# Kernel optimization log

Hardware: AMD Instinct MI355X
Metric: run time of the kernel (lower is better)

Reference implementation:

```python
import jax, jax.numpy as jnp
import numpy as np

N_NODES = 1_000_000
N_EDGES = 16_000_000
D = 2          # num_dimensions (hard-coded in source)
H = 64         # hidden_channnels
G = 1024       # number of graphs in the batch


def setup_inputs() -> dict:
    key = jax.random.key(0)
    ks = jax.random.split(key, 10)
    x = jax.random.normal(ks[0], (N_NODES, D), dtype=jnp.float32)
    edge_index = jax.random.randint(ks[1], (2, N_EDGES), 0, N_NODES, dtype=jnp.int64)
    batch = jnp.sort(jax.random.randint(ks[2], (N_NODES,), 0, G, dtype=jnp.int64))
    s = 0.5
    return {
        "x": x,
        "lin_w": jax.random.normal(ks[3], (D, D), dtype=jnp.float32) * s,
        "lin_b": jnp.zeros((D,), jnp.float32),
        "gn_weight": jnp.ones((D,), jnp.float32),
        "gn_bias": jnp.zeros((D,), jnp.float32),
        "gn_mean_scale": jnp.ones((D,), jnp.float32),
        "gcn_w": jax.random.normal(ks[4], (D, D), dtype=jnp.float32) * s,
        "gcn_b": jnp.zeros((D,), jnp.float32),
        "fc1_w": jax.random.normal(ks[5], (H, D), dtype=jnp.float32) * s,
        "fc1_b": jnp.zeros((H,), jnp.float32),
        "fc2_w": jax.random.normal(ks[6], (D, H), dtype=jnp.float32) * (1.0 / np.sqrt(H)),
        "fc2_b": jnp.zeros((D,), jnp.float32),
        "edge_index": edge_index,
        "batch": batch,
    }


def reference(x, lin_w, lin_b, gn_weight, gn_bias, gn_mean_scale,
              gcn_w, gcn_b, fc1_w, fc1_b, fc2_w, fc2_b, edge_index, batch):
    n = x.shape[0]
    # lin
    h = x @ lin_w.T + lin_b
    # GraphNorm called without batch -> single-graph stats; eps = num_dimensions = 2 (arg-order quirk)
    mean = h.mean(axis=0)
    out = h - mean * gn_mean_scale
    var = (out * out).mean(axis=0)
    h = gn_weight * out * jax.lax.rsqrt(var + jnp.float32(D)) + gn_bias
    h = jax.nn.relu(h)
    # GCNConv (add_self_loops=True, sym norm) + residual
    row, col = edge_index[0], edge_index[1]
    deg = jax.ops.segment_sum(jnp.ones_like(col, dtype=h.dtype), col, num_segments=n) + 1.0
    dis = jax.lax.rsqrt(deg)                       # deg^{-1/2}
    hw = h @ gcn_w.T                               # [N, D]
    msg = (dis[row] * dis[col])[:, None] * hw[row] # [E, D]
    agg = jax.ops.segment_sum(msg, col, num_segments=n)
    conv = agg + hw / deg[:, None] + gcn_b         # self-loop term = dis_i^2 * hw_i
    h = conv + h
    # fc1
    h = h @ fc1_w.T + fc1_b                        # [N, H]
    # InstanceNorm1d on 2D input -> unbatched (C=N, L=H): per-row norm over H; eps = H (arg-order quirk)
    m = h.mean(axis=1, keepdims=True)
    v = ((h - m) ** 2).mean(axis=1, keepdims=True)
    h = (h - m) * jax.lax.rsqrt(v + jnp.float32(H))
    # fc2
    h = h @ fc2_w.T + fc2_b                        # [N, D]
    # scatter_mean over batch
    ssum = jax.ops.segment_sum(h, batch, num_segments=G)
    cnt = jax.ops.segment_sum(jnp.ones((n,), h.dtype), batch, num_segments=G)
    return ssum / jnp.maximum(cnt, 1.0)[:, None]
```

## Files before the change

kernel.cpp:

```cpp
#include <hip/hip_runtime.h>

#define BLK 256
#define CH 8192
#define BSHIFT 12
#define BRANGE 4096
#define BMASK 4095
#define NSB 512


__global__ void k_stats(const float* __restrict__ x, int n, double* __restrict__ partials) {
    float s0 = 0.f, s1 = 0.f, s2 = 0.f, s3 = 0.f, s4 = 0.f;
    int nv = n >> 1;
    int stride = gridDim.x * blockDim.x;
    for (int i = blockIdx.x * blockDim.x + threadIdx.x; i < nv; i += stride) {
        float4 v = reinterpret_cast<const float4*>(x)[i];
        s0 += v.x + v.z; s1 += v.y + v.w;
        s2 += v.x * v.x + v.z * v.z;
        s3 += v.y * v.y + v.w * v.w;
        s4 += v.x * v.y + v.z * v.w;
    }
    if (blockIdx.x == 0 && threadIdx.x == 0 && (n & 1)) {
        float2 v = reinterpret_cast<const float2*>(x)[n - 1];
        s0 += v.x; s1 += v.y; s2 += v.x * v.x; s3 += v.y * v.y; s4 += v.x * v.y;
    }
    for (int off = 32; off; off >>= 1) {
        s0 += __shfl_down(s0, off);
        s1 += __shfl_down(s1, off);
        s2 += __shfl_down(s2, off);
        s3 += __shfl_down(s3, off);
        s4 += __shfl_down(s4, off);
    }
    __shared__ double lds[4][5];
    int wid = threadIdx.x >> 6;
    if ((threadIdx.x & 63) == 0) {
        lds[wid][0] = s0; lds[wid][1] = s1; lds[wid][2] = s2;
        lds[wid][3] = s3; lds[wid][4] = s4;
    }
    __syncthreads();
    if (threadIdx.x == 0) {
        double t0 = 0, t1 = 0, t2 = 0, t3 = 0, t4 = 0;
        for (int w = 0; w < 4; ++w) {
            t0 += lds[w][0]; t1 += lds[w][1]; t2 += lds[w][2];
            t3 += lds[w][3]; t4 += lds[w][4];
        }
        double* o = partials + (size_t)blockIdx.x * 5;
        o[0] = t0; o[1] = t1; o[2] = t2; o[3] = t3; o[4] = t4;
    }
}


__global__ void k_params(const double* __restrict__ partials, int np,
                         const int* __restrict__ bhist, int NB,
                         int* __restrict__ gbase, int* __restrict__ cursor,
                         const float* lin_w, const float* lin_b,
                         const float* gn_w, const float* gn_b, const float* gn_ms,
                         const float* gcn_w, const float* gcn_b,
                         const float* fc1_w, const float* fc1_b,
                         const float* fc2_w, const float* fc2_b,
                         int n, float* __restrict__ P) {
    int tid = threadIdx.x;
    if (bhist) {
        __shared__ int si[256];
        int hv = (tid < NB) ? bhist[tid] : 0;
        si[tid] = hv; __syncthreads();
        for (int off = 1; off < 256; off <<= 1) {
            int t = (tid >= off) ? si[tid - off] : 0;
            __syncthreads();
            si[tid] += t;
            __syncthreads();
        }
        if (tid < NB) { gbase[tid] = si[tid] - hv; cursor[tid] = si[tid] - hv; }
        if (tid == 0) gbase[NB] = si[255];
        __syncthreads();
    }
    double a0 = 0, a1 = 0, a2 = 0, a3 = 0, a4 = 0;
    for (int i = tid; i < np; i += blockDim.x) {
        const double* q = partials + (size_t)i * 5;
        a0 += q[0]; a1 += q[1]; a2 += q[2]; a3 += q[3]; a4 += q[4];
    }
    for (int off = 32; off; off >>= 1) {
        a0 += __shfl_down(a0, off);
        a1 += __shfl_down(a1, off);
        a2 += __shfl_down(a2, off);
        a3 += __shfl_down(a3, off);
        a4 += __shfl_down(a4, off);
    }
    __shared__ double red[4][5];
    int wid = tid >> 6;
    if ((tid & 63) == 0) {
        red[wid][0] = a0; red[wid][1] = a1; red[wid][2] = a2;
        red[wid][3] = a3; red[wid][4] = a4;
    }
    __syncthreads();
    if (tid != 0) return;
    double Sx0 = 0, Sx1 = 0, Sxx = 0, Syy = 0, Sxy = 0;
    for (int w = 0; w < 4; ++w) {
        Sx0 += red[w][0]; Sx1 += red[w][1]; Sxx += red[w][2];
        Syy += red[w][3]; Sxy += red[w][4];
    }
    double N = (double)n;
    for (int c = 0; c < 2; ++c) {
        double L0 = lin_w[c * 2], L1 = lin_w[c * 2 + 1], lb = lin_b[c];
        double m   = (L0 * Sx0 + L1 * Sx1) / N + lb;
        double Eh2 = (L0 * L0 * Sxx + L1 * L1 * Syy + 2.0 * L0 * L1 * Sxy
                      + 2.0 * lb * (L0 * Sx0 + L1 * Sx1)) / N + lb * lb;
        double s   = gn_ms[c];
        double var = Eh2 - 2.0 * s * m * m + s * s * m * m;
        double inv = 1.0 / sqrt(var + 2.0);
        double gam = gn_w[c];
        P[c * 2 + 0] = (float)(gam * inv * L0);
        P[c * 2 + 1] = (float)(gam * inv * L1);
        P[4 + c]     = (float)(gam * inv * (lb - m * s) + gn_b[c]);
    }
    P[6] = gcn_w[0]; P[7] = gcn_w[1]; P[8] = gcn_w[2]; P[9] = gcn_w[3];
    P[10] = gcn_b[0]; P[11] = gcn_b[1];
    double b0 = 0, b1 = 0, bb = 0;
    for (int j = 0; j < 64; ++j) { b0 += fc1_w[2 * j]; b1 += fc1_w[2 * j + 1]; bb += fc1_b[j]; }
    b0 /= 64.0; b1 /= 64.0; bb /= 64.0;
    double S00 = 0, S01 = 0, S11 = 0, Sb0 = 0, Sb1 = 0, Sbb = 0;
    double M00 = 0, M01 = 0, M10 = 0, M11 = 0, t0 = 0, t1 = 0;
    for (int j = 0; j < 64; ++j) {
        double w0 = fc1_w[2 * j] - b0, w1 = fc1_w[2 * j + 1] - b1, b = fc1_b[j] - bb;
        S00 += w0 * w0; S01 += w0 * w1; S11 += w1 * w1;
        Sb0 += w0 * b;  Sb1 += w1 * b;  Sbb += b * b;
        double f0 = fc2_w[j], f1 = fc2_w[64 + j];
        M00 += f0 * w0; M01 += f0 * w1; t0 += f0 * b;
        M10 += f1 * w0; M11 += f1 * w1; t1 += f1 * b;
    }
    P[12] = (float)(S00 / 64.0); P[13] = (float)(S01 / 64.0); P[14] = (float)(S11 / 64.0);
    P[15] = (float)(Sb0 / 64.0); P[16] = (float)(Sb1 / 64.0); P[17] = (float)(Sbb / 64.0);
    P[18] = (float)M00; P[19] = (float)M01; P[20] = (float)M10; P[21] = (float)M11;
    P[22] = (float)t0;  P[23] = (float)t1;
    P[24] = fc2_b[0];   P[25] = fc2_b[1];
}


__global__ void k_hist(const int* __restrict__ col, int E, int NB, int* __restrict__ bhist) {
    __shared__ int h[256];
    for (int j = threadIdx.x; j < 256; j += blockDim.x) h[j] = 0;
    __syncthreads();
    int nq = E >> 2;
    int stride = gridDim.x * blockDim.x;
    for (int q = blockIdx.x * blockDim.x + threadIdx.x; q < nq; q += stride) {
        int4 c = reinterpret_cast<const int4*>(col)[q];
        atomicAdd(&h[c.x >> BSHIFT], 1);
        atomicAdd(&h[c.y >> BSHIFT], 1);
        atomicAdd(&h[c.z >> BSHIFT], 1);
        atomicAdd(&h[c.w >> BSHIFT], 1);
    }
    if (blockIdx.x == 0) {
        for (int e = (nq << 2) + threadIdx.x; e < E; e += blockDim.x)
            atomicAdd(&h[col[e] >> BSHIFT], 1);
    }
    __syncthreads();
    for (int j = threadIdx.x; j < NB; j += blockDim.x)
        if (h[j]) atomicAdd(&bhist[j], h[j]);
}

__global__ __launch_bounds__(256) void k_binA(const int* __restrict__ row,
                                              const int* __restrict__ col, int E,
                                              int NB, int* __restrict__ cursor,
                                              unsigned* __restrict__ staging) {
    __shared__ unsigned buf[CH];
    __shared__ int h[256], si[256], lpos[256], lcur[256];
    int tid = threadIdx.x;
    int start = blockIdx.x * CH;
    int end = start + CH; if (end > E) end = E;
    h[tid] = 0;
    __syncthreads();
    for (int e = start + tid; e < end; e += 256)
        atomicAdd(&h[col[e] >> BSHIFT], 1);
    __syncthreads();
    int hv = h[tid];
    si[tid] = hv; __syncthreads();
    for (int off = 1; off < 256; off <<= 1) {
        int t = (tid >= off) ? si[tid - off] : 0;
        __syncthreads();
        si[tid] += t;
        __syncthreads();
    }
    lpos[tid] = si[tid] - hv;
    lcur[tid] = (tid < NB && hv) ? atomicAdd(&cursor[tid], hv) : 0;
    __syncthreads();
    for (int e = start + tid; e < end; e += 256) {
        int c = col[e];
        unsigned w = ((unsigned)row[e] << BSHIFT) | (unsigned)(c & BMASK);
        int slot = atomicAdd(&lpos[c >> BSHIFT], 1);
        buf[slot] = w;
    }
    __syncthreads();
    int wid = tid >> 6, lane = tid & 63;
    for (int b = wid; b < NB; b += 4) {
        int m = h[b];
        if (!m) continue;
        int lb = si[b] - m;
        int g = lcur[b];
        for (int k = lane; k < m; k += 64)
            staging[g + k] = buf[lb + k];
    }
}

__global__ __launch_bounds__(1024) void k_degprep(const unsigned* __restrict__ staging,
                                                  const int* __restrict__ gbase,
                                                  const float* __restrict__ x,
                                                  const float* __restrict__ P,
                                                  int n, int* __restrict__ deg,
                                                  float2* __restrict__ p) {
    __shared__ int hist[BRANGE];
    int tid = threadIdx.x;
    for (int j = tid; j < BRANGE; j += 1024) hist[j] = 0;
    __syncthreads();
    int s = gbase[blockIdx.x], e = gbase[blockIdx.x + 1];
    int pre = (4 - (s & 3)) & 3; int cnt = e - s; if (pre > cnt) pre = cnt;
    for (int i = s + tid; i < s + pre; i += 1024)
        atomicAdd(&hist[staging[i] & BMASK], 1);
    int vs = s + pre;
    int nq = (e - vs) >> 2;
    const uint4* sv = reinterpret_cast<const uint4*>(staging + vs);
    for (int q = tid; q < nq; q += 1024) {
        uint4 w = sv[q];
        atomicAdd(&hist[w.x & BMASK], 1);
        atomicAdd(&hist[w.y & BMASK], 1);
        atomicAdd(&hist[w.z & BMASK], 1);
        atomicAdd(&hist[w.w & BMASK], 1);
    }
    for (int i = vs + (nq << 2) + tid; i < e; i += 1024)
        atomicAdd(&hist[staging[i] & BMASK], 1);
    __syncthreads();
    float A00 = P[0], A01 = P[1], A10 = P[2], A11 = P[3], q0 = P[4], q1 = P[5];
    float g00 = P[6], g01 = P[7], g10 = P[8], g11 = P[9];
    int nb = blockIdx.x << BSHIFT;
    int lim = n - nb; if (lim > BRANGE) lim = BRANGE;
    for (int j = tid; j < lim; j += 1024) {
        int d = hist[j];
        deg[nb + j] = d;
        float2 v = reinterpret_cast<const float2*>(x)[nb + j];
        float gg0 = fmaxf(fmaf(A00, v.x, fmaf(A01, v.y, q0)), 0.f);
        float gg1 = fmaxf(fmaf(A10, v.x, fmaf(A11, v.y, q1)), 0.f);
        float hw0 = g00 * gg0 + g01 * gg1;
        float hw1 = g10 * gg0 + g11 * gg1;
        float degf = (float)d + 1.0f;
        float dis = rsqrtf(degf);
        p[nb + j] = make_float2(dis * hw0, dis * hw1);
    }
}

#define AGG2(W, PV) \
    atomicAdd(&acc[2 * ((W) & BMASK)],     (PV).x); \
    atomicAdd(&acc[2 * ((W) & BMASK) + 1], (PV).y);

__global__ __launch_bounds__(1024) void k_aggfin(
        const unsigned* __restrict__ staging, const int* __restrict__ gbase,
        const float2* __restrict__ p, const float* __restrict__ x,
        const int* __restrict__ deg, const int* __restrict__ batch,
        const float* __restrict__ Pp, int n,
        float* __restrict__ gsum, float* __restrict__ gcnt) {
    __shared__ float acc[2 * BRANGE];
    int tid = threadIdx.x;
    for (int j = tid; j < 2 * BRANGE; j += 1024) acc[j] = 0.f;
    __syncthreads();
    int s = gbase[blockIdx.x], e = gbase[blockIdx.x + 1];
    int cnt = e - s;
    int pre = (4 - (s & 3)) & 3; if (pre > cnt) pre = cnt;
    for (int i = s + tid; i < s + pre; i += 1024) {
        unsigned w = staging[i]; float2 pv = p[w >> BSHIFT];
        AGG2(w, pv)
    }
    int vs = s + pre;
    int nq = (e - vs) >> 2;
    const uint4* sv = reinterpret_cast<const uint4*>(staging + vs);
    int q = tid;
    for (; q + 3 * 1024 < nq; q += 4 * 1024) {
        uint4 wa = sv[q];
        uint4 wb = sv[q + 1024];
        uint4 wc = sv[q + 2048];
        uint4 wd = sv[q + 3072];
        float2 a0 = p[wa.x >> BSHIFT], a1 = p[wa.y >> BSHIFT];
        float2 a2 = p[wa.z >> BSHIFT], a3 = p[wa.w >> BSHIFT];
        float2 b0 = p[wb.x >> BSHIFT], b1 = p[wb.y >> BSHIFT];
        float2 b2 = p[wb.z >> BSHIFT], b3 = p[wb.w >> BSHIFT];
        float2 c0 = p[wc.x >> BSHIFT], c1 = p[wc.y >> BSHIFT];
        float2 c2 = p[wc.z >> BSHIFT], c3 = p[wc.w >> BSHIFT];
        float2 d0 = p[wd.x >> BSHIFT], d1 = p[wd.y >> BSHIFT];
        float2 d2 = p[wd.z >> BSHIFT], d3 = p[wd.w >> BSHIFT];
        AGG2(wa.x, a0) AGG2(wa.y, a1) AGG2(wa.z, a2) AGG2(wa.w, a3)
        AGG2(wb.x, b0) AGG2(wb.y, b1) AGG2(wb.z, b2) AGG2(wb.w, b3)
        AGG2(wc.x, c0) AGG2(wc.y, c1) AGG2(wc.z, c2) AGG2(wc.w, c3)
        AGG2(wd.x, d0) AGG2(wd.y, d1) AGG2(wd.z, d2) AGG2(wd.w, d3)
    }
    for (; q < nq; q += 1024) {
        uint4 w = sv[q];
        float2 p0 = p[w.x >> BSHIFT], p1 = p[w.y >> BSHIFT];
        float2 p2 = p[w.z >> BSHIFT], p3 = p[w.w >> BSHIFT];
        AGG2(w.x, p0) AGG2(w.y, p1) AGG2(w.z, p2) AGG2(w.w, p3)
    }
    for (int i = vs + (nq << 2) + tid; i < e; i += 1024) {
        unsigned w = staging[i]; float2 pv = p[w >> BSHIFT];
        AGG2(w, pv)
    }
    __syncthreads();

    float A00 = Pp[0], A01 = Pp[1], A10 = Pp[2], A11 = Pp[3], q0f = Pp[4], q1f = Pp[5];
    float g00 = Pp[6], g01 = Pp[7], g10 = Pp[8], g11 = Pp[9];
    float gb0 = Pp[10], gb1 = Pp[11];
    float S00 = Pp[12], S01 = Pp[13], S11 = Pp[14], Sb0 = Pp[15], Sb1 = Pp[16], Sbb = Pp[17];
    float M00 = Pp[18], M01 = Pp[19], M10 = Pp[20], M11 = Pp[21];
    float t0 = Pp[22], t1 = Pp[23], fb0 = Pp[24], fb1 = Pp[25];
    int nb = blockIdx.x << BSHIFT;
    int lim = n - nb; if (lim > BRANGE) lim = BRANGE;
    for (int j = tid; j < lim; j += 1024) {
        int i = nb + j;
        float2 v = reinterpret_cast<const float2*>(x)[i];
        float g0 = fmaxf(fmaf(A00, v.x, fmaf(A01, v.y, q0f)), 0.f);
        float g1 = fmaxf(fmaf(A10, v.x, fmaf(A11, v.y, q1f)), 0.f);
        float hw0 = g00 * g0 + g01 * g1;
        float hw1 = g10 * g0 + g11 * g1;
        float degf = (float)deg[i] + 1.0f;
        float dis = rsqrtf(degf);
        float a0v = acc[2 * j], a1v = acc[2 * j + 1];
        float c0 = dis * a0v + hw0 / degf + gb0 + g0;
        float c1 = dis * a1v + hw1 / degf + gb1 + g1;
        float vq = S00 * c0 * c0 + 2.f * S01 * c0 * c1 + S11 * c1 * c1
                 + 2.f * Sb0 * c0 + 2.f * Sb1 * c1 + Sbb;
        float inv = rsqrtf(vq + 64.0f);
        float o0 = inv * (M00 * c0 + M01 * c1 + t0) + fb0;
        float o1 = inv * (M10 * c0 + M11 * c1 + t1) + fb1;
        int bg = batch[i];
        unsigned long long act = __ballot(true);
        if (act == ~0ull) {
            int b0 = __shfl(bg, 0);
            if (__all(bg == b0)) {
                float s0 = o0, s1 = o1;
                for (int off = 32; off; off >>= 1) {
                    s0 += __shfl_down(s0, off);
                    s1 += __shfl_down(s1, off);
                }
                if ((tid & 63) == 0) {
                    atomicAdd(&gsum[2 * b0], s0);
                    atomicAdd(&gsum[2 * b0 + 1], s1);
                    atomicAdd(&gcnt[b0], 64.0f);
                }
            } else {
                atomicAdd(&gsum[2 * bg], o0);
                atomicAdd(&gsum[2 * bg + 1], o1);
                atomicAdd(&gcnt[bg], 1.0f);
            }
        } else {
            atomicAdd(&gsum[2 * bg], o0);
            atomicAdd(&gsum[2 * bg + 1], o1);
            atomicAdd(&gcnt[bg], 1.0f);
        }
    }
}

__global__ void k_div(const float* __restrict__ gsum, const float* __restrict__ gcnt,
                      float* __restrict__ out, int G) {
    int g = blockIdx.x * blockDim.x + threadIdx.x;
    if (g < G) {
        float c = fmaxf(gcnt[g], 1.0f);
        out[2 * g]     = gsum[2 * g] / c;
        out[2 * g + 1] = gsum[2 * g + 1] / c;
    }
}


__global__ void k_prep(const float* __restrict__ x, const int* __restrict__ deg,
                       const float* __restrict__ P, int n, float2* __restrict__ p) {
    int stride = gridDim.x * blockDim.x;
    float A00 = P[0], A01 = P[1], A10 = P[2], A11 = P[3], q0 = P[4], q1 = P[5];
    float g00 = P[6], g01 = P[7], g10 = P[8], g11 = P[9];
    for (int i = blockIdx.x * blockDim.x + threadIdx.x; i < n; i += stride) {
        float2 v = reinterpret_cast<const float2*>(x)[i];
        float g0 = fmaxf(fmaf(A00, v.x, fmaf(A01, v.y, q0)), 0.f);
        float g1 = fmaxf(fmaf(A10, v.x, fmaf(A11, v.y, q1)), 0.f);
        float hw0 = g00 * g0 + g01 * g1;
        float hw1 = g10 * g0 + g11 * g1;
        float degf = (float)deg[i] + 1.0f;
        float dis = rsqrtf(degf);
        p[i] = make_float2(dis * hw0, dis * hw1);
    }
}

__global__ void k_deg(const int* __restrict__ col, int E, int* __restrict__ deg) {
    int nq = (E + 3) >> 2;
    int q = blockIdx.x * blockDim.x + threadIdx.x;
    if (q >= nq) return;
    int base = q << 2;
    if (base + 3 < E) {
        int4 c = reinterpret_cast<const int4*>(col)[q];
        atomicAdd(&deg[c.x], 1); atomicAdd(&deg[c.y], 1);
        atomicAdd(&deg[c.z], 1); atomicAdd(&deg[c.w], 1);
    } else {
        for (int e = base; e < E; ++e) atomicAdd(&deg[col[e]], 1);
    }
}

__global__ void k_edge(const int* __restrict__ row, const int* __restrict__ col, int E,
                       const float2* __restrict__ p, float* __restrict__ agg) {
    int nq = (E + 3) >> 2;
    int q = blockIdx.x * blockDim.x + threadIdx.x;
    if (q >= nq) return;
    int base = q << 2;
    if (base + 3 < E) {
        int4 r = reinterpret_cast<const int4*>(row)[q];
        int4 c = reinterpret_cast<const int4*>(col)[q];
        float2 p0 = p[r.x], p1 = p[r.y], p2 = p[r.z], p3 = p[r.w];
        atomicAdd(&agg[2 * c.x], p0.x); atomicAdd(&agg[2 * c.x + 1], p0.y);
        atomicAdd(&agg[2 * c.y], p1.x); atomicAdd(&agg[2 * c.y + 1], p1.y);
        atomicAdd(&agg[2 * c.z], p2.x); atomicAdd(&agg[2 * c.z + 1], p2.y);
        atomicAdd(&agg[2 * c.w], p3.x); atomicAdd(&agg[2 * c.w + 1], p3.y);
    } else {
        for (int e = base; e < E; ++e) {
            float2 pv = p[row[e]];
            atomicAdd(&agg[2 * col[e]], pv.x);
            atomicAdd(&agg[2 * col[e] + 1], pv.y);
        }
    }
}

__global__ void k_final(const float* __restrict__ x, const int* __restrict__ deg,
                        const float* __restrict__ agg, const int* __restrict__ batch,
                        const float* __restrict__ P, int n,
                        float* __restrict__ gsum, float* __restrict__ gcnt) {
    int i = blockIdx.x * blockDim.x + threadIdx.x;
    bool valid = i < n;
    float A00 = P[0], A01 = P[1], A10 = P[2], A11 = P[3], q0 = P[4], q1 = P[5];
    float g00 = P[6], g01 = P[7], g10 = P[8], g11 = P[9];
    float gb0 = P[10], gb1 = P[11];
    float S00 = P[12], S01 = P[13], S11 = P[14], Sb0 = P[15], Sb1 = P[16], Sbb = P[17];
    float M00 = P[18], M01 = P[19], M10 = P[20], M11 = P[21];
    float t0 = P[22], t1 = P[23], fb0 = P[24], fb1 = P[25];

    float o0 = 0.f, o1 = 0.f;
    int b = 0;
    if (valid) {
        float2 v = reinterpret_cast<const float2*>(x)[i];
        float g0 = fmaxf(fmaf(A00, v.x, fmaf(A01, v.y, q0)), 0.f);
        float g1 = fmaxf(fmaf(A10, v.x, fmaf(A11, v.y, q1)), 0.f);
        float hw0 = g00 * g0 + g01 * g1;
        float hw1 = g10 * g0 + g11 * g1;
        float degf = (float)deg[i] + 1.0f;
        float dis = rsqrtf(degf);
        float a0 = agg[2 * i], a1 = agg[2 * i + 1];
        float c0 = dis * a0 + hw0 / degf + gb0 + g0;
        float c1 = dis * a1 + hw1 / degf + gb1 + g1;
        float vq = S00 * c0 * c0 + 2.f * S01 * c0 * c1 + S11 * c1 * c1
                 + 2.f * Sb0 * c0 + 2.f * Sb1 * c1 + Sbb;
        float inv = rsqrtf(vq + 64.0f);
        o0 = inv * (M00 * c0 + M01 * c1 + t0) + fb0;
        o1 = inv * (M10 * c0 + M11 * c1 + t1) + fb1;
        b = batch[i];
    }
    unsigned long long act = __ballot(valid);
    if (act == ~0ull) {
        int b0 = __shfl(b, 0);
        if (__all(b == b0)) {
            float s0 = o0, s1 = o1;
            for (int off = 32; off; off >>= 1) {
                s0 += __shfl_down(s0, off);
                s1 += __shfl_down(s1, off);
            }
            if ((threadIdx.x & 63) == 0) {
                atomicAdd(&gsum[2 * b0], s0);
                atomicAdd(&gsum[2 * b0 + 1], s1);
                atomicAdd(&gcnt[b0], 64.0f);
            }
        } else {
            atomicAdd(&gsum[2 * b], o0);
            atomicAdd(&gsum[2 * b + 1], o1);
            atomicAdd(&gcnt[b], 1.0f);
        }
    } else if (valid) {
        atomicAdd(&gsum[2 * b], o0);
        atomicAdd(&gsum[2 * b + 1], o1);
        atomicAdd(&gcnt[b], 1.0f);
    }
}


extern "C" void kernel_launch(void* const* d_in, const int* in_sizes, int n_in,
                              void* d_out, int out_size, void* d_ws, size_t ws_size,
                              hipStream_t stream) {
    const float* x      = (const float*)d_in[0];
    const float* lin_w  = (const float*)d_in[1];
    const float* lin_b  = (const float*)d_in[2];
    const float* gn_w   = (const float*)d_in[3];
    const float* gn_b   = (const float*)d_in[4];
    const float* gn_ms  = (const float*)d_in[5];
    const float* gcn_w  = (const float*)d_in[6];
    const float* gcn_b  = (const float*)d_in[7];
    const float* fc1_w  = (const float*)d_in[8];
    const float* fc1_b  = (const float*)d_in[9];
    const float* fc2_w  = (const float*)d_in[10];
    const float* fc2_b  = (const float*)d_in[11];
    const int*   ei     = (const int*)d_in[12];
    const int*   batch  = (const int*)d_in[13];

    int n = in_sizes[0] / 2;
    int E = in_sizes[12] / 2;
    int G = out_size / 2;
    const int* row = ei;
    const int* col = ei + E;

    char* ws = (char*)d_ws;
    int nb_nodes = (n + BLK - 1) / BLK;
    int NB = (n + BRANGE - 1) >> BSHIFT;

    size_t zero_end  = 16384 + (size_t)12 * G;
    size_t part_off  = (zero_end + 255) & ~(size_t)255;
    size_t deg_off   = (part_off + (size_t)40 * NSB + 255) & ~(size_t)255;
    size_t p_off     = deg_off + (size_t)4 * n;
    size_t stag_off  = p_off + (size_t)8 * n;
    size_t need      = stag_off + (size_t)4 * E;

    bool fast = (n <= (1 << 20)) && (NB <= 253) && (need <= ws_size) &&
                (zero_end <= 16384 + 12288);

    if (fast) {
        float*    P       = (float*)(ws + 64);
        int*      bhist   = (int*)(ws + 4096);
        int*      gbase   = (int*)(ws + 8192);
        int*      cursor  = (int*)(ws + 12288);
        float*    gsum    = (float*)(ws + 16384);
        float*    gcnt    = (float*)(ws + 16384 + (size_t)8 * G);
        double*   part    = (double*)(ws + part_off);
        int*      deg     = (int*)(ws + deg_off);
        float2*   p       = (float2*)(ws + p_off);
        unsigned* staging = (unsigned*)(ws + stag_off);

        hipMemsetAsync(d_ws, 0, zero_end, stream);

        int nbinA = (E + CH - 1) / CH;

        k_stats<<<NSB, BLK, 0, stream>>>(x, n, part);
        k_hist<<<512, BLK, 0, stream>>>(col, E, NB, bhist);
        k_params<<<1, 256, 0, stream>>>(part, NSB, bhist, NB, gbase, cursor,
                                        lin_w, lin_b, gn_w, gn_b, gn_ms,
                                        gcn_w, gcn_b, fc1_w, fc1_b, fc2_w, fc2_b, n, P);
        k_binA<<<nbinA, 256, 0, stream>>>(row, col, E, NB, cursor, staging);
        k_degprep<<<NB, 1024, 0, stream>>>(staging, gbase, x, P, n, deg, p);
        k_aggfin<<<NB, 1024, 0, stream>>>(staging, gbase, p, x, deg, batch,
                                          P, n, gsum, gcnt);
        k_div<<<(G + BLK - 1) / BLK, BLK, 0, stream>>>(gsum, gcnt, (float*)d_out, G);
    } else {
        float*  P     = (float*)(ws + 64);
        float*  gsum  = (float*)(ws + 4096);
        float*  gcnt  = (float*)(ws + 4096 + (size_t)8 * G);
        size_t fzero_end = 4096 + (size_t)12 * G;
        size_t fpart_off = (fzero_end + 255) & ~(size_t)255;
        size_t fdeg_off  = (fpart_off + (size_t)40 * NSB + 255) & ~(size_t)255;
        int*    deg   = (int*)(ws + fdeg_off);
        size_t fagg_off = fdeg_off + (size_t)4 * n;
        float*  agg   = (float*)(ws + fagg_off);
        size_t fp_off = fagg_off + (size_t)8 * n;
        float2* p     = (float2*)(ws + fp_off);
        double* part  = (double*)(ws + fpart_off);

        hipMemsetAsync(ws + 4096, 0, fzero_end - 4096, stream);
        hipMemsetAsync(ws + fdeg_off, 0, (size_t)12 * n, stream);

        int nq = (E + 3) >> 2;
        int nb_edge = (nq + BLK - 1) / BLK;

        k_stats<<<NSB, BLK, 0, stream>>>(x, n, part);
        k_deg<<<nb_edge, BLK, 0, stream>>>(col, E, deg);
        k_params<<<1, 256, 0, stream>>>(part, NSB, (const int*)nullptr, 0,
                                        (int*)nullptr, (int*)nullptr,
                                        lin_w, lin_b, gn_w, gn_b, gn_ms,
                                        gcn_w, gcn_b, fc1_w, fc1_b, fc2_w, fc2_b, n, P);
        k_prep<<<nb_nodes, BLK, 0, stream>>>(x, deg, P, n, p);
        k_edge<<<nb_edge, BLK, 0, stream>>>(row, col, E, p, agg);
        k_final<<<nb_nodes, BLK, 0, stream>>>(x, deg, agg, batch, P, n, gsum, gcnt);
        k_div<<<(G + BLK - 1) / BLK, BLK, 0, stream>>>(gsum, gcnt, (float*)d_out, G);
    }
}
```

Baseline: 370.6 us.

## Fuse stats with histogram and split aggregation across two blocks per bucket

```diff
diff --git a/kernel.cpp b/kernel.cpp
--- a/kernel.cpp
+++ b/kernel.cpp
@@ -8,11 +8,31 @@
 #define NSB 512
 
 
-__global__ void k_stats(const float* __restrict__ x, int n, double* __restrict__ partials) {
+__global__ void k_stats_hist(const float* __restrict__ x, int n,
+                             const int* __restrict__ col, int E, int NB,
+                             double* __restrict__ partials, int* __restrict__ bhist) {
+    __shared__ int h[256];
+    for (int j = threadIdx.x; j < 256; j += blockDim.x) h[j] = 0;
+    __syncthreads();
+    int stride = gridDim.x * blockDim.x;
+    int gtid = blockIdx.x * blockDim.x + threadIdx.x;
+
+    int nqe = E >> 2;
+    for (int q = gtid; q < nqe; q += stride) {
+        int4 c = reinterpret_cast<const int4*>(col)[q];
+        atomicAdd(&h[c.x >> BSHIFT], 1);
+        atomicAdd(&h[c.y >> BSHIFT], 1);
+        atomicAdd(&h[c.z >> BSHIFT], 1);
+        atomicAdd(&h[c.w >> BSHIFT], 1);
+    }
+    if (blockIdx.x == 0) {
+        for (int e = (nqe << 2) + threadIdx.x; e < E; e += blockDim.x)
+            atomicAdd(&h[col[e] >> BSHIFT], 1);
+    }
+
     float s0 = 0.f, s1 = 0.f, s2 = 0.f, s3 = 0.f, s4 = 0.f;
     int nv = n >> 1;
-    int stride = gridDim.x * blockDim.x;
-    for (int i = blockIdx.x * blockDim.x + threadIdx.x; i < nv; i += stride) {
+    for (int i = gtid; i < nv; i += stride) {
         float4 v = reinterpret_cast<const float4*>(x)[i];
         s0 += v.x + v.z; s1 += v.y + v.w;
         s2 += v.x * v.x + v.z * v.z;
@@ -46,6 +66,8 @@
         double* o = partials + (size_t)blockIdx.x * 5;
         o[0] = t0; o[1] = t1; o[2] = t2; o[3] = t3; o[4] = t4;
     }
+    for (int j = threadIdx.x; j < NB; j += blockDim.x)
+        if (h[j]) atomicAdd(&bhist[j], h[j]);
 }
 
 
@@ -249,17 +271,18 @@
     atomicAdd(&acc[2 * ((W) & BMASK)],     (PV).x); \
     atomicAdd(&acc[2 * ((W) & BMASK) + 1], (PV).y);
 
-__global__ __launch_bounds__(1024) void k_aggfin(
+__global__ __launch_bounds__(1024) void k_agg(
         const unsigned* __restrict__ staging, const int* __restrict__ gbase,
-        const float2* __restrict__ p, const float* __restrict__ x,
-        const int* __restrict__ deg, const int* __restrict__ batch,
-        const float* __restrict__ Pp, int n,
-        float* __restrict__ gsum, float* __restrict__ gcnt) {
+        const float2* __restrict__ p, float* __restrict__ pacc) {
     __shared__ float acc[2 * BRANGE];
     int tid = threadIdx.x;
     for (int j = tid; j < 2 * BRANGE; j += 1024) acc[j] = 0.f;
     __syncthreads();
-    int s = gbase[blockIdx.x], e = gbase[blockIdx.x + 1];
+    int b = blockIdx.x >> 1, half = blockIdx.x & 1;
+    int s0 = gbase[b], e0 = gbase[b + 1];
+    int hc = (e0 - s0) >> 1;
+    int s = s0 + half * hc;
+    int e = half ? e0 : (s0 + hc);
     int cnt = e - s;
     int pre = (4 - (s & 3)) & 3; if (pre > cnt) pre = cnt;
     for (int i = s + tid; i < s + pre; i += 1024) {
@@ -299,17 +322,31 @@
         AGG2(w, pv)
     }
     __syncthreads();
-
+    float* pa = pacc + (size_t)blockIdx.x * (2 * BRANGE);
+    for (int j = tid; j < 2 * BRANGE; j += 1024) pa[j] = acc[j];
+}
+
+__global__ __launch_bounds__(1024) void k_fin(
+        const float* __restrict__ pacc, const float* __restrict__ x,
+        const int* __restrict__ deg, const int* __restrict__ batch,
+        const float* __restrict__ Pp, int n,
+        float* __restrict__ gsum, float* __restrict__ gcnt) {
+    int tid = threadIdx.x;
+    int b = blockIdx.x;
+    const float2* a0p = reinterpret_cast<const float2*>(pacc + (size_t)(2 * b)     * (2 * BRANGE));
+    const float2* a1p = reinterpret_cast<const float2*>(pacc + (size_t)(2 * b + 1) * (2 * BRANGE));
     float A00 = Pp[0], A01 = Pp[1], A10 = Pp[2], A11 = Pp[3], q0f = Pp[4], q1f = Pp[5];
     float g00 = Pp[6], g01 = Pp[7], g10 = Pp[8], g11 = Pp[9];
     float gb0 = Pp[10], gb1 = Pp[11];
     float S00 = Pp[12], S01 = Pp[13], S11 = Pp[14], Sb0 = Pp[15], Sb1 = Pp[16], Sbb = Pp[17];
     float M00 = Pp[18], M01 = Pp[19], M10 = Pp[20], M11 = Pp[21];
     float t0 = Pp[22], t1 = Pp[23], fb0 = Pp[24], fb1 = Pp[25];
-    int nb = blockIdx.x << BSHIFT;
+    int nb = b << BSHIFT;
     int lim = n - nb; if (lim > BRANGE) lim = BRANGE;
     for (int j = tid; j < lim; j += 1024) {
         int i = nb + j;
+        float2 A = a0p[j], B = a1p[j];
+        float a0v = A.x + B.x, a1v = A.y + B.y;
         float2 v = reinterpret_cast<const float2*>(x)[i];
         float g0 = fmaxf(fmaf(A00, v.x, fmaf(A01, v.y, q0f)), 0.f);
         float g1 = fmaxf(fmaf(A10, v.x, fmaf(A11, v.y, q1f)), 0.f);
@@ -317,7 +354,6 @@
         float hw1 = g10 * g0 + g11 * g1;
         float degf = (float)deg[i] + 1.0f;
         float dis = rsqrtf(degf);
-        float a0v = acc[2 * j], a1v = acc[2 * j + 1];
         float c0 = dis * a0v + hw0 / degf + gb0 + g0;
         float c1 = dis * a1v + hw1 / degf + gb1 + g1;
         float vq = S00 * c0 * c0 + 2.f * S01 * c0 * c1 + S11 * c1 * c1
@@ -326,24 +362,17 @@
         float o0 = inv * (M00 * c0 + M01 * c1 + t0) + fb0;
         float o1 = inv * (M10 * c0 + M11 * c1 + t1) + fb1;
         int bg = batch[i];
-        unsigned long long act = __ballot(true);
-        if (act == ~0ull) {
-            int b0 = __shfl(bg, 0);
-            if (__all(bg == b0)) {
-                float s0 = o0, s1 = o1;
-                for (int off = 32; off; off >>= 1) {
-                    s0 += __shfl_down(s0, off);
-                    s1 += __shfl_down(s1, off);
-                }
-                if ((tid & 63) == 0) {
-                    atomicAdd(&gsum[2 * b0], s0);
-                    atomicAdd(&gsum[2 * b0 + 1], s1);
-                    atomicAdd(&gcnt[b0], 64.0f);
-                }
-            } else {
-                atomicAdd(&gsum[2 * bg], o0);
-                atomicAdd(&gsum[2 * bg + 1], o1);
-                atomicAdd(&gcnt[bg], 1.0f);
+        int b0 = __shfl(bg, 0);
+        if (__all(bg == b0)) {
+            float s0 = o0, s1 = o1;
+            for (int off = 32; off; off >>= 1) {
+                s0 += __shfl_down(s0, off);
+                s1 += __shfl_down(s1, off);
+            }
+            if ((tid & 63) == 0) {
+                atomicAdd(&gsum[2 * b0], s0);
+                atomicAdd(&gsum[2 * b0 + 1], s1);
+                atomicAdd(&gcnt[b0], 64.0f);
             }
         } else {
             atomicAdd(&gsum[2 * bg], o0);
@@ -363,6 +392,46 @@
     }
 }
 
+
+__global__ void k_stats(const float* __restrict__ x, int n, double* __restrict__ partials) {
+    float s0 = 0.f, s1 = 0.f, s2 = 0.f, s3 = 0.f, s4 = 0.f;
+    int nv = n >> 1;
+    int stride = gridDim.x * blockDim.x;
+    for (int i = blockIdx.x * blockDim.x + threadIdx.x; i < nv; i += stride) {
+        float4 v = reinterpret_cast<const float4*>(x)[i];
+        s0 += v.x + v.z; s1 += v.y + v.w;
+        s2 += v.x * v.x + v.z * v.z;
+        s3 += v.y * v.y + v.w * v.w;
+        s4 += v.x * v.y + v.z * v.w;
+    }
+    if (blockIdx.x == 0 && threadIdx.x == 0 && (n & 1)) {
+        float2 v = reinterpret_cast<const float2*>(x)[n - 1];
+        s0 += v.x; s1 += v.y; s2 += v.x * v.x; s3 += v.y * v.y; s4 += v.x * v.y;
+    }
+    for (int off = 32; off; off >>= 1) {
+        s0 += __shfl_down(s0, off);
+        s1 += __shfl_down(s1, off);
+        s2 += __shfl_down(s2, off);
+        s3 += __shfl_down(s3, off);
+        s4 += __shfl_down(s4, off);
+    }
+    __shared__ double lds[4][5];
+    int wid = threadIdx.x >> 6;
+    if ((threadIdx.x & 63) == 0) {
+        lds[wid][0] = s0; lds[wid][1] = s1; lds[wid][2] = s2;
+        lds[wid][3] = s3; lds[wid][4] = s4;
+    }
+    __syncthreads();
+    if (threadIdx.x == 0) {
+        double t0 = 0, t1 = 0, t2 = 0, t3 = 0, t4 = 0;
+        for (int w = 0; w < 4; ++w) {
+            t0 += lds[w][0]; t1 += lds[w][1]; t2 += lds[w][2];
+            t3 += lds[w][3]; t4 += lds[w][4];
+        }
+        double* o = partials + (size_t)blockIdx.x * 5;
+        o[0] = t0; o[1] = t1; o[2] = t2; o[3] = t3; o[4] = t4;
+    }
+}
 
 __global__ void k_prep(const float* __restrict__ x, const int* __restrict__ deg,
                        const float* __restrict__ P, int n, float2* __restrict__ p) {
@@ -510,7 +579,8 @@
     size_t part_off  = (zero_end + 255) & ~(size_t)255;
     size_t deg_off   = (part_off + (size_t)40 * NSB + 255) & ~(size_t)255;
     size_t p_off     = deg_off + (size_t)4 * n;
-    size_t stag_off  = p_off + (size_t)8 * n;
+    size_t pacc_off  = p_off + (size_t)8 * n;
+    size_t stag_off  = pacc_off + (size_t)NB * 2 * (2 * BRANGE) * 4;
     size_t need      = stag_off + (size_t)4 * E;
 
     bool fast = (n <= (1 << 20)) && (NB <= 253) && (need <= ws_size) &&
@@ -526,21 +596,21 @@
         double*   part    = (double*)(ws + part_off);
         int*      deg     = (int*)(ws + deg_off);
         float2*   p       = (float2*)(ws + p_off);
+        float*    pacc    = (float*)(ws + pacc_off);
         unsigned* staging = (unsigned*)(ws + stag_off);
 
         hipMemsetAsync(d_ws, 0, zero_end, stream);
 
         int nbinA = (E + CH - 1) / CH;
 
-        k_stats<<<NSB, BLK, 0, stream>>>(x, n, part);
-        k_hist<<<512, BLK, 0, stream>>>(col, E, NB, bhist);
+        k_stats_hist<<<NSB, BLK, 0, stream>>>(x, n, col, E, NB, part, bhist);
         k_params<<<1, 256, 0, stream>>>(part, NSB, bhist, NB, gbase, cursor,
                                         lin_w, lin_b, gn_w, gn_b, gn_ms,
                                         gcn_w, gcn_b, fc1_w, fc1_b, fc2_w, fc2_b, n, P);
         k_binA<<<nbinA, 256, 0, stream>>>(row, col, E, NB, cursor, staging);
         k_degprep<<<NB, 1024, 0, stream>>>(staging, gbase, x, P, n, deg, p);
-        k_aggfin<<<NB, 1024, 0, stream>>>(staging, gbase, p, x, deg, batch,
-                                          P, n, gsum, gcnt);
+        k_agg<<<NB * 2, 1024, 0, stream>>>(staging, gbase, p, pacc);
+        k_fin<<<NB, 1024, 0, stream>>>(pacc, x, deg, batch, P, n, gsum, gcnt);
         k_div<<<(G + BLK - 1) / BLK, BLK, 0, stream>>>(gsum, gcnt, (float*)d_out, G);
     } else {
         float*  P     = (float*)(ws + 64);
```

Result: no change. 377.8 us (+1.9%).

## Sub-bucket edges by source-row segment to improve gather locality in aggregation

Applied to the files above, without the earlier changes.

```diff
diff --git a/kernel.cpp b/kernel.cpp
--- a/kernel.cpp
+++ b/kernel.cpp
@@ -5,14 +5,38 @@
 #define BSHIFT 12
 #define BRANGE 4096
 #define BMASK 4095
+#define NSEG 4
 #define NSB 512
 
 
-__global__ void k_stats(const float* __restrict__ x, int n, double* __restrict__ partials) {
+__global__ void k_stats_hist(const float* __restrict__ x, int n,
+                             const int* __restrict__ row, const int* __restrict__ col,
+                             int E, int NB, int NKEY, int segshift,
+                             double* __restrict__ partials, int* __restrict__ bhist) {
+    __shared__ int h[1024];
+    for (int j = threadIdx.x; j < 1024; j += blockDim.x) h[j] = 0;
+    __syncthreads();
+    int stride = gridDim.x * blockDim.x;
+    int gtid = blockIdx.x * blockDim.x + threadIdx.x;
+
+    int nqe = E >> 2;
+    const int4* rv = reinterpret_cast<const int4*>(row);
+    const int4* cv = reinterpret_cast<const int4*>(col);
+    for (int q = gtid; q < nqe; q += stride) {
+        int4 r = rv[q]; int4 c = cv[q];
+        atomicAdd(&h[(r.x >> segshift) * NB + (c.x >> BSHIFT)], 1);
+        atomicAdd(&h[(r.y >> segshift) * NB + (c.y >> BSHIFT)], 1);
+        atomicAdd(&h[(r.z >> segshift) * NB + (c.z >> BSHIFT)], 1);
+        atomicAdd(&h[(r.w >> segshift) * NB + (c.w >> BSHIFT)], 1);
+    }
+    if (blockIdx.x == 0) {
+        for (int e = (nqe << 2) + threadIdx.x; e < E; e += blockDim.x)
+            atomicAdd(&h[(row[e] >> segshift) * NB + (col[e] >> BSHIFT)], 1);
+    }
+
     float s0 = 0.f, s1 = 0.f, s2 = 0.f, s3 = 0.f, s4 = 0.f;
     int nv = n >> 1;
-    int stride = gridDim.x * blockDim.x;
-    for (int i = blockIdx.x * blockDim.x + threadIdx.x; i < nv; i += stride) {
+    for (int i = gtid; i < nv; i += stride) {
         float4 v = reinterpret_cast<const float4*>(x)[i];
         s0 += v.x + v.z; s1 += v.y + v.w;
         s2 += v.x * v.x + v.z * v.z;
@@ -46,11 +70,13 @@
         double* o = partials + (size_t)blockIdx.x * 5;
         o[0] = t0; o[1] = t1; o[2] = t2; o[3] = t3; o[4] = t4;
     }
+    for (int j = threadIdx.x; j < NKEY; j += blockDim.x)
+        if (h[j]) atomicAdd(&bhist[j], h[j]);
 }
 
 
 __global__ void k_params(const double* __restrict__ partials, int np,
-                         const int* __restrict__ bhist, int NB,
+                         const int* __restrict__ bhist, int NKEY,
                          int* __restrict__ gbase, int* __restrict__ cursor,
                          const float* lin_w, const float* lin_b,
                          const float* gn_w, const float* gn_b, const float* gn_ms,
@@ -61,16 +87,25 @@
     int tid = threadIdx.x;
     if (bhist) {
         __shared__ int si[256];
-        int hv = (tid < NB) ? bhist[tid] : 0;
-        si[tid] = hv; __syncthreads();
+        int b4 = tid * 4;
+        int v0 = (b4     < NKEY) ? bhist[b4]     : 0;
+        int v1 = (b4 + 1 < NKEY) ? bhist[b4 + 1] : 0;
+        int v2 = (b4 + 2 < NKEY) ? bhist[b4 + 2] : 0;
+        int v3 = (b4 + 3 < NKEY) ? bhist[b4 + 3] : 0;
+        int sum = v0 + v1 + v2 + v3;
+        si[tid] = sum; __syncthreads();
         for (int off = 1; off < 256; off <<= 1) {
             int t = (tid >= off) ? si[tid - off] : 0;
             __syncthreads();
             si[tid] += t;
             __syncthreads();
         }
-        if (tid < NB) { gbase[tid] = si[tid] - hv; cursor[tid] = si[tid] - hv; }
-        if (tid == 0) gbase[NB] = si[255];
+        int base = si[tid] - sum;
+        if (b4     < NKEY) { gbase[b4]     = base;            cursor[b4]     = base; }
+        if (b4 + 1 < NKEY) { gbase[b4 + 1] = base + v0;       cursor[b4 + 1] = base + v0; }
+        if (b4 + 2 < NKEY) { gbase[b4 + 2] = base + v0 + v1;  cursor[b4 + 2] = base + v0 + v1; }
+        if (b4 + 3 < NKEY) { gbase[b4 + 3] = base + v0 + v1 + v2; cursor[b4 + 3] = base + v0 + v1 + v2; }
+        if (tid == 255) gbase[NKEY] = si[255];
         __syncthreads();
     }
     double a0 = 0, a1 = 0, a2 = 0, a3 = 0, a4 = 0;
@@ -135,82 +170,63 @@
 }
 
 
-__global__ void k_hist(const int* __restrict__ col, int E, int NB, int* __restrict__ bhist) {
-    __shared__ int h[256];
-    for (int j = threadIdx.x; j < 256; j += blockDim.x) h[j] = 0;
-    __syncthreads();
-    int nq = E >> 2;
-    int stride = gridDim.x * blockDim.x;
-    for (int q = blockIdx.x * blockDim.x + threadIdx.x; q < nq; q += stride) {
-        int4 c = reinterpret_cast<const int4*>(col)[q];
-        atomicAdd(&h[c.x >> BSHIFT], 1);
-        atomicAdd(&h[c.y >> BSHIFT], 1);
-        atomicAdd(&h[c.z >> BSHIFT], 1);
-        atomicAdd(&h[c.w >> BSHIFT], 1);
-    }
-    if (blockIdx.x == 0) {
-        for (int e = (nq << 2) + threadIdx.x; e < E; e += blockDim.x)
-            atomicAdd(&h[col[e] >> BSHIFT], 1);
-    }
-    __syncthreads();
-    for (int j = threadIdx.x; j < NB; j += blockDim.x)
-        if (h[j]) atomicAdd(&bhist[j], h[j]);
-}
-
 __global__ __launch_bounds__(256) void k_binA(const int* __restrict__ row,
                                               const int* __restrict__ col, int E,
-                                              int NB, int* __restrict__ cursor,
+                                              int NB, int NKEY, int segshift,
+                                              int* __restrict__ cursor,
                                               unsigned* __restrict__ staging) {
     __shared__ unsigned buf[CH];
-    __shared__ int h[256], si[256], lpos[256], lcur[256];
+    __shared__ int h[1024], bb[1024], lcur[1024];
+    __shared__ int si[256];
     int tid = threadIdx.x;
     int start = blockIdx.x * CH;
     int end = start + CH; if (end > E) end = E;
-    h[tid] = 0;
+    for (int j = tid; j < 1024; j += 256) h[j] = 0;
     __syncthreads();
     for (int e = start + tid; e < end; e += 256)
-        atomicAdd(&h[col[e] >> BSHIFT], 1);
-    __syncthreads();
-    int hv = h[tid];
-    si[tid] = hv; __syncthreads();
+        atomicAdd(&h[(row[e] >> segshift) * NB + (col[e] >> BSHIFT)], 1);
+    __syncthreads();
+    int b4 = tid * 4;
+    int v0 = h[b4], v1 = h[b4 + 1], v2 = h[b4 + 2], v3 = h[b4 + 3];
+    int sum = v0 + v1 + v2 + v3;
+    si[tid] = sum; __syncthreads();
     for (int off = 1; off < 256; off <<= 1) {
         int t = (tid >= off) ? si[tid - off] : 0;
         __syncthreads();
         si[tid] += t;
         __syncthreads();
     }
-    lpos[tid] = si[tid] - hv;
-    lcur[tid] = (tid < NB && hv) ? atomicAdd(&cursor[tid], hv) : 0;
+    int base = si[tid] - sum;
+    bb[b4]     = base;
+    bb[b4 + 1] = base + v0;
+    bb[b4 + 2] = base + v0 + v1;
+    bb[b4 + 3] = base + v0 + v1 + v2;
+    lcur[b4]     = (b4     < NKEY && v0) ? atomicAdd(&cursor[b4],     v0) : 0;
+    lcur[b4 + 1] = (b4 + 1 < NKEY && v1) ? atomicAdd(&cursor[b4 + 1], v1) : 0;
+    lcur[b4 + 2] = (b4 + 2 < NKEY && v2) ? atomicAdd(&cursor[b4 + 2], v2) : 0;
+    lcur[b4 + 3] = (b4 + 3 < NKEY && v3) ? atomicAdd(&cursor[b4 + 3], v3) : 0;
     __syncthreads();
     for (int e = start + tid; e < end; e += 256) {
-        int c = col[e];
-        unsigned w = ((unsigned)row[e] << BSHIFT) | (unsigned)(c & BMASK);
-        int slot = atomicAdd(&lpos[c >> BSHIFT], 1);
+        int r = row[e], c = col[e];
+        int key = (r >> segshift) * NB + (c >> BSHIFT);
+        unsigned w = ((unsigned)r << BSHIFT) | (unsigned)(c & BMASK);
+        int slot = atomicAdd(&bb[key], 1);
         buf[slot] = w;
     }
     __syncthreads();
     int wid = tid >> 6, lane = tid & 63;
-    for (int b = wid; b < NB; b += 4) {
-        int m = h[b];
+    for (int k = wid; k < NKEY; k += 4) {
+        int m = h[k];
         if (!m) continue;
-        int lb = si[b] - m;
-        int g = lcur[b];
-        for (int k = lane; k < m; k += 64)
-            staging[g + k] = buf[lb + k];
-    }
-}
-
-__global__ __launch_bounds__(1024) void k_degprep(const unsigned* __restrict__ staging,
-                                                  const int* __restrict__ gbase,
-                                                  const float* __restrict__ x,
-                                                  const float* __restrict__ P,
-                                                  int n, int* __restrict__ deg,
-                                                  float2* __restrict__ p) {
-    __shared__ int hist[BRANGE];
-    int tid = threadIdx.x;
-    for (int j = tid; j < BRANGE; j += 1024) hist[j] = 0;
-    __syncthreads();
-    int s = gbase[blockIdx.x], e = gbase[blockIdx.x + 1];
+        int lb = bb[k] - m;
+        int g = lcur[k];
+        for (int j = lane; j < m; j += 64)
+            staging[g + j] = buf[lb + j];
+    }
+}
+
+__device__ __forceinline__ void hist_range(const unsigned* __restrict__ staging,
+                                           int s, int e, int* hist, int tid) {
     int pre = (4 - (s & 3)) & 3; int cnt = e - s; if (pre > cnt) pre = cnt;
     for (int i = s + tid; i < s + pre; i += 1024)
         atomicAdd(&hist[staging[i] & BMASK], 1);
@@ -226,6 +242,22 @@
     }
     for (int i = vs + (nq << 2) + tid; i < e; i += 1024)
         atomicAdd(&hist[staging[i] & BMASK], 1);
+}
+
+__global__ __launch_bounds__(1024) void k_degprep(const unsigned* __restrict__ staging,
+                                                  const int* __restrict__ gbase,
+                                                  const float* __restrict__ x,
+                                                  const float* __restrict__ P,
+                                                  int n, int NB, int* __restrict__ deg,
+                                                  float2* __restrict__ p) {
+    __shared__ int hist[BRANGE];
+    int tid = threadIdx.x;
+    for (int j = tid; j < BRANGE; j += 1024) hist[j] = 0;
+    __syncthreads();
+    for (int s = 0; s < NSEG; ++s) {
+        int idx = s * NB + blockIdx.x;
+        hist_range(staging, gbase[idx], gbase[idx + 1], hist, tid);
+    }
     __syncthreads();
     float A00 = P[0], A01 = P[1], A10 = P[2], A11 = P[3], q0 = P[4], q1 = P[5];
     float g00 = P[6], g01 = P[7], g10 = P[8], g11 = P[9];
@@ -253,50 +285,53 @@
         const unsigned* __restrict__ staging, const int* __restrict__ gbase,
         const float2* __restrict__ p, const float* __restrict__ x,
         const int* __restrict__ deg, const int* __restrict__ batch,
-        const float* __restrict__ Pp, int n,
+        const float* __restrict__ Pp, int n, int NB,
         float* __restrict__ gsum, float* __restrict__ gcnt) {
     __shared__ float acc[2 * BRANGE];
     int tid = threadIdx.x;
     for (int j = tid; j < 2 * BRANGE; j += 1024) acc[j] = 0.f;
     __syncthreads();
-    int s = gbase[blockIdx.x], e = gbase[blockIdx.x + 1];
-    int cnt = e - s;
-    int pre = (4 - (s & 3)) & 3; if (pre > cnt) pre = cnt;
-    for (int i = s + tid; i < s + pre; i += 1024) {
-        unsigned w = staging[i]; float2 pv = p[w >> BSHIFT];
-        AGG2(w, pv)
-    }
-    int vs = s + pre;
-    int nq = (e - vs) >> 2;
-    const uint4* sv = reinterpret_cast<const uint4*>(staging + vs);
-    int q = tid;
-    for (; q + 3 * 1024 < nq; q += 4 * 1024) {
-        uint4 wa = sv[q];
-        uint4 wb = sv[q + 1024];
-        uint4 wc = sv[q + 2048];
-        uint4 wd = sv[q + 3072];
-        float2 a0 = p[wa.x >> BSHIFT], a1 = p[wa.y >> BSHIFT];
-        float2 a2 = p[wa.z >> BSHIFT], a3 = p[wa.w >> BSHIFT];
-        float2 b0 = p[wb.x >> BSHIFT], b1 = p[wb.y >> BSHIFT];
-        float2 b2 = p[wb.z >> BSHIFT], b3 = p[wb.w >> BSHIFT];
-        float2 c0 = p[wc.x >> BSHIFT], c1 = p[wc.y >> BSHIFT];
-        float2 c2 = p[wc.z >> BSHIFT], c3 = p[wc.w >> BSHIFT];
-        float2 d0 = p[wd.x >> BSHIFT], d1 = p[wd.y >> BSHIFT];
-        float2 d2 = p[wd.z >> BSHIFT], d3 = p[wd.w >> BSHIFT];
-        AGG2(wa.x, a0) AGG2(wa.y, a1) AGG2(wa.z, a2) AGG2(wa.w, a3)
-        AGG2(wb.x, b0) AGG2(wb.y, b1) AGG2(wb.z, b2) AGG2(wb.w, b3)
-        AGG2(wc.x, c0) AGG2(wc.y, c1) AGG2(wc.z, c2) AGG2(wc.w, c3)
-        AGG2(wd.x, d0) AGG2(wd.y, d1) AGG2(wd.z, d2) AGG2(wd.w, d3)
-    }
-    for (; q < nq; q += 1024) {
-        uint4 w = sv[q];
-        float2 p0 = p[w.x >> BSHIFT], p1 = p[w.y >> BSHIFT];
-        float2 p2 = p[w.z >> BSHIFT], p3 = p[w.w >> BSHIFT];
-        AGG2(w.x, p0) AGG2(w.y, p1) AGG2(w.z, p2) AGG2(w.w, p3)
-    }
-    for (int i = vs + (nq << 2) + tid; i < e; i += 1024) {
-        unsigned w = staging[i]; float2 pv = p[w >> BSHIFT];
-        AGG2(w, pv)
+    for (int s = 0; s < NSEG; ++s) {
+        int idx = s * NB + blockIdx.x;
+        int rs = gbase[idx], re = gbase[idx + 1];
+        int cnt = re - rs;
+        int pre = (4 - (rs & 3)) & 3; if (pre > cnt) pre = cnt;
+        for (int i = rs + tid; i < rs + pre; i += 1024) {
+            unsigned w = staging[i]; float2 pv = p[w >> BSHIFT];
+            AGG2(w, pv)
+        }
+        int vs = rs + pre;
+        int nq = (re - vs) >> 2;
+        const uint4* sv = reinterpret_cast<const uint4*>(staging + vs);
+        int qtr = nq >> 2;
+        for (int q = tid; q < qtr; q += 1024) {
+            uint4 wa = sv[q];
+            uint4 wb = sv[q + qtr];
+            uint4 wc = sv[q + 2 * qtr];
+            uint4 wd = sv[q + 3 * qtr];
+            float2 a0 = p[wa.x >> BSHIFT], a1 = p[wa.y >> BSHIFT];
+            float2 a2 = p[wa.z >> BSHIFT], a3 = p[wa.w >> BSHIFT];
+            float2 b0 = p[wb.x >> BSHIFT], b1 = p[wb.y >> BSHIFT];
+            float2 b2 = p[wb.z >> BSHIFT], b3 = p[wb.w >> BSHIFT];
+            float2 c0 = p[wc.x >> BSHIFT], c1 = p[wc.y >> BSHIFT];
+            float2 c2 = p[wc.z >> BSHIFT], c3 = p[wc.w >> BSHIFT];
+            float2 d0 = p[wd.x >> BSHIFT], d1 = p[wd.y >> BSHIFT];
+            float2 d2 = p[wd.z >> BSHIFT], d3 = p[wd.w >> BSHIFT];
+            AGG2(wa.x, a0) AGG2(wa.y, a1) AGG2(wa.z, a2) AGG2(wa.w, a3)
+            AGG2(wb.x, b0) AGG2(wb.y, b1) AGG2(wb.z, b2) AGG2(wb.w, b3)
+            AGG2(wc.x, c0) AGG2(wc.y, c1) AGG2(wc.z, c2) AGG2(wc.w, c3)
+            AGG2(wd.x, d0) AGG2(wd.y, d1) AGG2(wd.z, d2) AGG2(wd.w, d3)
+        }
+        for (int q = (qtr << 2) + tid; q < nq; q += 1024) {
+            uint4 w = sv[q];
+            float2 p0 = p[w.x >> BSHIFT], p1 = p[w.y >> BSHIFT];
+            float2 p2 = p[w.z >> BSHIFT], p3 = p[w.w >> BSHIFT];
+            AGG2(w.x, p0) AGG2(w.y, p1) AGG2(w.z, p2) AGG2(w.w, p3)
+        }
+        for (int i = vs + (nq << 2) + tid; i < re; i += 1024) {
+            unsigned w = staging[i]; float2 pv = p[w >> BSHIFT];
+            AGG2(w, pv)
+        }
     }
     __syncthreads();
 
@@ -364,6 +399,46 @@
 }
 
 
+__global__ void k_stats(const float* __restrict__ x, int n, double* __restrict__ partials) {
+    float s0 = 0.f, s1 = 0.f, s2 = 0.f, s3 = 0.f, s4 = 0.f;
+    int nv = n >> 1;
+    int stride = gridDim.x * blockDim.x;
+    for (int i = blockIdx.x * blockDim.x + threadIdx.x; i < nv; i += stride) {
+        float4 v = reinterpret_cast<const float4*>(x)[i];
+        s0 += v.x + v.z; s1 += v.y + v.w;
+        s2 += v.x * v.x + v.z * v.z;
+        s3 += v.y * v.y + v.w * v.w;
+        s4 += v.x * v.y + v.z * v.w;
+    }
+    if (blockIdx.x == 0 && threadIdx.x == 0 && (n & 1)) {
+        float2 v = reinterpret_cast<const float2*>(x)[n - 1];
+        s0 += v.x; s1 += v.y; s2 += v.x * v.x; s3 += v.y * v.y; s4 += v.x * v.y;
+    }
+    for (int off = 32; off; off >>= 1) {
+        s0 += __shfl_down(s0, off);
+        s1 += __shfl_down(s1, off);
+        s2 += __shfl_down(s2, off);
+        s3 += __shfl_down(s3, off);
+        s4 += __shfl_down(s4, off);
+    }
+    __shared__ double lds[4][5];
+    int wid = threadIdx.x >> 6;
+    if ((threadIdx.x & 63) == 0) {
+        lds[wid][0] = s0; lds[wid][1] = s1; lds[wid][2] = s2;
+        lds[wid][3] = s3; lds[wid][4] = s4;
+    }
+    __syncthreads();
+    if (threadIdx.x == 0) {
+        double t0 = 0, t1 = 0, t2 = 0, t3 = 0, t4 = 0;
+        for (int w = 0; w < 4; ++w) {
+            t0 += lds[w][0]; t1 += lds[w][1]; t2 += lds[w][2];
+            t3 += lds[w][3]; t4 += lds[w][4];
+        }
+        double* o = partials + (size_t)blockIdx.x * 5;
+        o[0] = t0; o[1] = t1; o[2] = t2; o[3] = t3; o[4] = t4;
+    }
+}
+
 __global__ void k_prep(const float* __restrict__ x, const int* __restrict__ deg,
                        const float* __restrict__ P, int n, float2* __restrict__ p) {
     int stride = gridDim.x * blockDim.x;
@@ -505,6 +580,9 @@
     char* ws = (char*)d_ws;
     int nb_nodes = (n + BLK - 1) / BLK;
     int NB = (n + BRANGE - 1) >> BSHIFT;
+    int NKEY = NSEG * NB;
+    int segshift = 0;
+    while (((unsigned)(n - 1) >> segshift) >= (unsigned)NSEG) ++segshift;
 
     size_t zero_end  = 16384 + (size_t)12 * G;
     size_t part_off  = (zero_end + 255) & ~(size_t)255;
@@ -513,7 +591,8 @@
     size_t stag_off  = p_off + (size_t)8 * n;
     size_t need      = stag_off + (size_t)4 * E;
 
-    bool fast = (n <= (1 << 20)) && (NB <= 253) && (need <= ws_size) &&
+    bool fast = (n <= (1 << 20)) && (NB <= 253) && (NKEY <= 1020) &&
+                ((E & 3) == 0) && (need <= ws_size) &&
                 (zero_end <= 16384 + 12288);
 
     if (fast) {
@@ -532,15 +611,16 @@
 
         int nbinA = (E + CH - 1) / CH;
 
-        k_stats<<<NSB, BLK, 0, stream>>>(x, n, part);
-        k_hist<<<512, BLK, 0, stream>>>(col, E, NB, bhist);
-        k_params<<<1, 256, 0, stream>>>(part, NSB, bhist, NB, gbase, cursor,
+        k_stats_hist<<<NSB, BLK, 0, stream>>>(x, n, row, col, E, NB, NKEY, segshift,
+                                              part, bhist);
+        k_params<<<1, 256, 0, stream>>>(part, NSB, bhist, NKEY, gbase, cursor,
                                         lin_w, lin_b, gn_w, gn_b, gn_ms,
                                         gcn_w, gcn_b, fc1_w, fc1_b, fc2_w, fc2_b, n, P);
-        k_binA<<<nbinA, 256, 0, stream>>>(row, col, E, NB, cursor, staging);
-        k_degprep<<<NB, 1024, 0, stream>>>(staging, gbase, x, P, n, deg, p);
+        k_binA<<<nbinA, 256, 0, stream>>>(row, col, E, NB, NKEY, segshift,
+                                          cursor, staging);
+        k_degprep<<<NB, 1024, 0, stream>>>(staging, gbase, x, P, n, NB, deg, p);
         k_aggfin<<<NB, 1024, 0, stream>>>(staging, gbase, p, x, deg, batch,
-                                          P, n, gsum, gcnt);
+                                          P, n, NB, gsum, gcnt);
         k_div<<<(G + BLK - 1) / BLK, BLK, 0, stream>>>(gsum, gcnt, (float*)d_out, G);
     } else {
         float*  P     = (float*)(ws + 64);
```

Result: slower. 586.6 us (+58.3%).
